# Performance work log

Hardware: AMD Instinct MI355X
Metric: run time of the kernel (lower is better)

The kernel has to match this reference:

```python
import jax, jax.numpy as jnp
import numpy as np

ALPHA = 0.5
PATH_LEN = 7  # 1 start entity + 3 (module, entity) hops
NUM_ENTITIES = 200000
EMBED = 128
NUM_MOD = 64
HIDDEN = 512
OUT_DIM = 64
BATCH = 8192


def setup_inputs() -> dict:
    key = jax.random.key(0)
    ks = jax.random.split(key, 8)
    stdv = 1.0 / np.sqrt(EMBED)
    return {
        "entity_embeds": jax.random.normal(ks[0], (NUM_ENTITIES, EMBED), jnp.float32) * 0.05,
        "W_mods": jax.random.uniform(ks[1], (NUM_MOD, EMBED, EMBED), jnp.float32, -stdv, stdv),
        "W1": jax.random.normal(ks[2], (HIDDEN, EMBED), jnp.float32) * stdv,
        "b1": jax.random.normal(ks[3], (HIDDEN,), jnp.float32) * 0.01,
        "W2": jax.random.normal(ks[4], (OUT_DIM, HIDDEN), jnp.float32) * (1.0 / np.sqrt(HIDDEN)),
        "b2": jax.random.normal(ks[5], (OUT_DIM,), jnp.float32) * 0.01,
        "entity_ids": jax.random.randint(ks[6], (BATCH, 4), 0, NUM_ENTITIES, jnp.int64 if jax.config.jax_enable_x64 else jnp.int32),
        "module_ids": jax.random.randint(ks[7], (BATCH, 3), 0, NUM_MOD, jnp.int64 if jax.config.jax_enable_x64 else jnp.int32),
    }


def reference(entity_embeds, W_mods, W1, b1, W2, b2, entity_ids, module_ids):
    # Batched version of ModuleNet.forward over a batch of fixed-length-7 paths.
    x = entity_embeds[entity_ids[:, 0]]  # [B, E] start entity embedding
    bias = x
    for h in range(3):  # hops over (module_id, entity_id) pairs
        Wm = W_mods[module_ids[:, h]]          # [B, E, E] per-row weight gather
        bias = entity_embeds[entity_ids[:, h + 1]]  # [B, E]
        x = jax.nn.relu(jnp.einsum('boi,bi->bo', Wm, x) + bias)
    w = 1.0 / (PATH_LEN * ALPHA)
    out = (1.0 - w) * bias + w * x  # [B, E]
    # classifier: Linear -> ReLU -> Linear
    h1 = jax.nn.relu(out @ W1.T + b1)
    logits = h1 @ W2.T + b2  # [B, OUT_DIM]
    return logits
```

## Files before the change

kernel.cpp:

```cpp
#include <hip/hip_runtime.h>

namespace {

typedef short bf16x8 __attribute__((ext_vector_type(8)));
typedef float f32x4 __attribute__((ext_vector_type(4)));

constexpr int BATCH = 8192;
constexpr int NMOD  = 64;
constexpr int CAP   = 256;
constexpr int CSTR  = 16;
constexpr float WB  = 1.0f / (7.0f * 0.5f);

constexpr size_t OFF_XH0 = 0;
constexpr size_t OFF_XL0 = 524288;
constexpr size_t OFF_XH1 = 1048576;
constexpr size_t OFF_XL1 = 1572864;
constexpr size_t OFF_W1H = 2097152;
constexpr size_t OFF_W1L = 2129920;
constexpr size_t OFF_W2H = 2162688;
constexpr size_t OFF_W2L = 2179072;
constexpr size_t OFF_CNT = 2195456;
constexpr size_t OFF_BKT = 2198528;

__device__ __forceinline__ ushort f2bf(float x) {
  unsigned u = __builtin_bit_cast(unsigned, x);
  u += 0x7FFFu + ((u >> 16) & 1u);
  return (ushort)(u >> 16);
}
__device__ __forceinline__ float bf2f(ushort h) {
  return __builtin_bit_cast(float, ((unsigned)h) << 16);
}
__device__ __forceinline__ void cvt8(const float* v, bf16x8& hi, bf16x8& lo) {
#pragma unroll
  for (int j = 0; j < 8; ++j) {
    const float x = v[j];
    const ushort h = f2bf(x);
    hi[j] = (short)h;
    lo[j] = (short)f2bf(x - bf2f(h));
  }
}

__global__ __launch_bounds__(256) void k_prep(const float* __restrict__ W1,
                                              const float* __restrict__ W2,
                                              const int* __restrict__ mids,
                                              float* __restrict__ ws) {
  __shared__ int wsum[4];
  const int bx = blockIdx.x;
  const int tid = threadIdx.x;
  if (bx < 48) {
    const float* src;
    ushort *dh, *dl;
    size_t i8;
    if (bx < 32) {
      src = W1; dh = (ushort*)(ws + OFF_W1H); dl = (ushort*)(ws + OFF_W1L);
      i8 = (size_t)bx * 256 + tid;
    } else {
      src = W2; dh = (ushort*)(ws + OFF_W2H); dl = (ushort*)(ws + OFF_W2L);
      i8 = (size_t)(bx - 32) * 256 + tid;
    }
    float v[8];
    *(float4*)&v[0] = *(const float4*)&src[i8 * 8];
    *(float4*)&v[4] = *(const float4*)&src[i8 * 8 + 4];
    bf16x8 hi, lo;
    cvt8(v, hi, lo);
    *(bf16x8*)&dh[i8 * 8] = hi;
    *(bf16x8*)&dl[i8 * 8] = lo;
  } else {
    const int hm = bx - 48;
    const int h = hm >> 6, m = hm & 63;
    int* cnt = (int*)(ws + OFF_CNT);
    int* bkt = (int*)(ws + OFF_BKT) + hm * CAP;
    const int wv = tid >> 6, ln = tid & 63;
    int count = 0;
    for (int it = 0; it < BATCH / 256; ++it) {
      const int b = it * 256 + tid;
      const bool hit = (mids[b * 3 + h] == m);
      const unsigned long long mask = __ballot(hit);
      const int pre = __popcll(mask & ((1ull << ln) - 1ull));
      if (ln == 0) wsum[wv] = __popcll(mask);
      __syncthreads();
      int wbase = count;
#pragma unroll
      for (int u = 0; u < 4; ++u)
        if (u < wv) wbase += wsum[u];
      if (hit) bkt[wbase + pre] = b;
      count += wsum[0] + wsum[1] + wsum[2] + wsum[3];
      __syncthreads();
    }
    if (tid == 0) cnt[hm * CSTR] = count;
  }
}

template <int HOP>
__global__ __launch_bounds__(256, 2) void k_hop(const float* __restrict__ E,
                                                const float* __restrict__ Wm,
                                                const int* __restrict__ eids,
                                                float* __restrict__ ws) {
  const int m = blockIdx.x >> 2, sl = blockIdx.x & 3;
  const int cn = ((const int*)(ws + OFF_CNT))[(HOP * NMOD + m) * CSTR];
  const int r0 = sl * 64;
  if (r0 >= cn) return;
  const int nr = min(64, cn - r0);

  __shared__ ushort wh[128 * 72];
  __shared__ ushort wl[128 * 72];
  __shared__ int rows[64], esrc[64], ebia[64];

  const int tid = threadIdx.x;
  const float* WmG = Wm + (size_t)m * 16384;
  const int* bkt = (const int*)(ws + OFF_BKT) + (HOP * NMOD + m) * CAP + r0;
  const ushort* XHp = (const ushort*)(ws + (HOP == 2 ? OFF_XH1 : OFF_XH0));
  const ushort* XLp = (const ushort*)(ws + (HOP == 2 ? OFF_XL1 : OFF_XL0));
  ushort* XHn = (ushort*)(ws + (HOP == 1 ? OFF_XH1 : OFF_XH0));
  ushort* XLn = (ushort*)(ws + (HOP == 1 ? OFF_XL1 : OFF_XL0));

  if (tid < 64) {
    const int b = bkt[tid < nr ? tid : 0];
    rows[tid] = b;
    esrc[tid] = (HOP == 0) ? eids[b * 4] : b;
    ebia[tid] = eids[b * 4 + HOP + 1];
  }

  const int w = tid >> 6, l = tid & 63;
  const int lg = l >> 4, lr = l & 15;
  const int g0 = (w & 1) * 2, f0 = (w >> 1) * 4;

  f32x4 acc[2][4] = {};

#pragma unroll
  for (int p = 0; p < 2; ++p) {
    __syncthreads();
    for (int e = tid; e < 128 * 8; e += 256) {
      const int c = e >> 3, s = e & 7;
      float v[8];
      const float* sp = &WmG[(size_t)c * 128 + p * 64 + s * 8];
      *(float4*)&v[0] = *(const float4*)&sp[0];
      *(float4*)&v[4] = *(const float4*)&sp[4];
      bf16x8 hi, lo;
      cvt8(v, hi, lo);
      *(bf16x8*)&wh[c * 72 + s * 8] = hi;
      *(bf16x8*)&wl[c * 72 + s * 8] = lo;
    }
    __syncthreads();

    bf16x8 ah[2][2], al[2][2];
#pragma unroll
    for (int g = 0; g < 2; ++g) {
      const int row = (g0 + g) * 16 + lr;
#pragma unroll
      for (int s = 0; s < 2; ++s) {
        const int k0 = p * 64 + s * 32 + lg * 8;
        if (HOP == 0) {
          const float* sp = E + (size_t)esrc[row] * 128;
          float v[8];
          *(float4*)&v[0] = *(const float4*)&sp[k0];
          *(float4*)&v[4] = *(const float4*)&sp[k0 + 4];
          cvt8(v, ah[g][s], al[g][s]);
        } else {
          const size_t xo = (size_t)esrc[row] * 128 + k0;
          ah[g][s] = *(const bf16x8*)&XHp[xo];
          al[g][s] = *(const bf16x8*)&XLp[xo];
        }
      }
    }

#pragma unroll
    for (int f = 0; f < 4; ++f) {
      const int c = (f0 + f) * 16 + lr;
#pragma unroll
      for (int s = 0; s < 2; ++s) {
        const bf16x8 bh = *(const bf16x8*)&wh[c * 72 + s * 32 + lg * 8];
        const bf16x8 bl = *(const bf16x8*)&wl[c * 72 + s * 32 + lg * 8];
#pragma unroll
        for (int g = 0; g < 2; ++g) {
          acc[g][f] = __builtin_amdgcn_mfma_f32_16x16x32_bf16(ah[g][s], bh, acc[g][f], 0, 0, 0);
          acc[g][f] = __builtin_amdgcn_mfma_f32_16x16x32_bf16(al[g][s], bh, acc[g][f], 0, 0, 0);
          acc[g][f] = __builtin_amdgcn_mfma_f32_16x16x32_bf16(ah[g][s], bl, acc[g][f], 0, 0, 0);
        }
      }
    }
  }

#pragma unroll
  for (int g = 0; g < 2; ++g) {
#pragma unroll
    for (int q = 0; q < 4; ++q) {
      const int row = (g0 + g) * 16 + lg * 4 + q;
      if (row < nr) {
        const int b = rows[row];
        const float* bp = E + (size_t)ebia[row] * 128;
        const size_t ob = (size_t)b * 128;
#pragma unroll
        for (int f = 0; f < 4; ++f) {
          const int col = (f0 + f) * 16 + lr;
          const float bias = bp[col];
          float v = fmaxf(acc[g][f][q] + bias, 0.f);
          if (HOP == 2) v = (1.f - WB) * bias + WB * v;
          const ushort h = f2bf(v);
          XHn[ob + col] = h;
          XLn[ob + col] = f2bf(v - bf2f(h));
        }
      }
    }
  }
}

constexpr int HSTR = 520;
__global__ __launch_bounds__(256, 2) void k_mlp(const float* __restrict__ b1,
                                                const float* __restrict__ b2,
                                                float* __restrict__ ws,
                                                float* __restrict__ out) {
  __shared__ ushort hh[16 * HSTR];
  __shared__ ushort hl[16 * HSTR];
  const int tid = threadIdx.x;
  const int row0 = blockIdx.x * 16;
  const ushort* XH = (const ushort*)(ws + OFF_XH0);
  const ushort* XL = (const ushort*)(ws + OFF_XL0);
  const ushort* W1H = (const ushort*)(ws + OFF_W1H);
  const ushort* W1L = (const ushort*)(ws + OFF_W1L);
  const ushort* W2H = (const ushort*)(ws + OFF_W2H);
  const ushort* W2L = (const ushort*)(ws + OFF_W2L);

  const int w = tid >> 6, l = tid & 63;
  const int lg = l >> 4, lr = l & 15;

  bf16x8 ah[4], al[4];
#pragma unroll
  for (int s = 0; s < 4; ++s) {
    const size_t xo = (size_t)(row0 + lr) * 128 + s * 32 + lg * 8;
    ah[s] = *(const bf16x8*)&XH[xo];
    al[s] = *(const bf16x8*)&XL[xo];
  }
  f32x4 acc[8] = {};
#pragma unroll
  for (int f = 0; f < 8; ++f) {
    const int c = w * 128 + f * 16 + lr;
#pragma unroll
    for (int s = 0; s < 4; ++s) {
      const size_t wo = (size_t)c * 128 + s * 32 + lg * 8;
      const bf16x8 bh = *(const bf16x8*)&W1H[wo];
      const bf16x8 bl = *(const bf16x8*)&W1L[wo];
      acc[f] = __builtin_amdgcn_mfma_f32_16x16x32_bf16(ah[s], bh, acc[f], 0, 0, 0);
      acc[f] = __builtin_amdgcn_mfma_f32_16x16x32_bf16(al[s], bh, acc[f], 0, 0, 0);
      acc[f] = __builtin_amdgcn_mfma_f32_16x16x32_bf16(ah[s], bl, acc[f], 0, 0, 0);
    }
  }
#pragma unroll
  for (int f = 0; f < 8; ++f) {
    const int c = w * 128 + f * 16 + lr;
    const float bb = b1[c];
#pragma unroll
    for (int q = 0; q < 4; ++q) {
      const int r = lg * 4 + q;
      const float v = fmaxf(acc[f][q] + bb, 0.f);
      const ushort h = f2bf(v);
      hh[r * HSTR + c] = h;
      hl[r * HSTR + c] = f2bf(v - bf2f(h));
    }
  }
  __syncthreads();

  f32x4 acc2 = {};
#pragma unroll 4
  for (int s = 0; s < 16; ++s) {
    const size_t wo = (size_t)(w * 16 + lr) * 512 + s * 32 + lg * 8;
    const bf16x8 a2h = *(const bf16x8*)&W2H[wo];
    const bf16x8 a2l = *(const bf16x8*)&W2L[wo];
    const int ko = s * 32 + lg * 8;
    const bf16x8 b2h = *(const bf16x8*)&hh[lr * HSTR + ko];
    const bf16x8 b2l = *(const bf16x8*)&hl[lr * HSTR + ko];
    acc2 = __builtin_amdgcn_mfma_f32_16x16x32_bf16(a2h, b2h, acc2, 0, 0, 0);
    acc2 = __builtin_amdgcn_mfma_f32_16x16x32_bf16(a2l, b2h, acc2, 0, 0, 0);
    acc2 = __builtin_amdgcn_mfma_f32_16x16x32_bf16(a2h, b2l, acc2, 0, 0, 0);
  }
  const float4 bb2 = *(const float4*)&b2[w * 16 + lg * 4];
  float4 o;
  o.x = acc2[0] + bb2.x;
  o.y = acc2[1] + bb2.y;
  o.z = acc2[2] + bb2.z;
  o.w = acc2[3] + bb2.w;
  *(float4*)&out[(size_t)(row0 + lr) * 64 + w * 16 + lg * 4] = o;
}

}

extern "C" void kernel_launch(void* const* d_in, const int* in_sizes, int n_in,
                              void* d_out, int out_size, void* d_ws,
                              size_t ws_size, hipStream_t stream) {
  const float* E  = (const float*)d_in[0];
  const float* Wm = (const float*)d_in[1];
  const float* W1 = (const float*)d_in[2];
  const float* b1 = (const float*)d_in[3];
  const float* W2 = (const float*)d_in[4];
  const float* b2 = (const float*)d_in[5];
  const int* eids = (const int*)d_in[6];
  const int* mids = (const int*)d_in[7];
  float* out = (float*)d_out;
  float* ws = (float*)d_ws;

  k_prep<<<dim3(240), dim3(256), 0, stream>>>(W1, W2, mids, ws);
  k_hop<0><<<dim3(256), dim3(256), 0, stream>>>(E, Wm, eids, ws);
  k_hop<1><<<dim3(256), dim3(256), 0, stream>>>(E, Wm, eids, ws);
  k_hop<2><<<dim3(256), dim3(256), 0, stream>>>(E, Wm, eids, ws);
  k_mlp<<<dim3(512), dim3(256), 0, stream>>>(b1, b2, ws, out);
}
```

Before: 85.79 us.

## Pre-split module weights to bf16 hi/lo once and halve hop output columns per block

```diff
diff --git a/kernel.cpp b/kernel.cpp
--- a/kernel.cpp
+++ b/kernel.cpp
@@ -11,16 +11,18 @@
 constexpr int CSTR  = 16;
 constexpr float WB  = 1.0f / (7.0f * 0.5f);
 
-constexpr size_t OFF_XH0 = 0;
-constexpr size_t OFF_XL0 = 524288;
-constexpr size_t OFF_XH1 = 1048576;
-constexpr size_t OFF_XL1 = 1572864;
-constexpr size_t OFF_W1H = 2097152;
-constexpr size_t OFF_W1L = 2129920;
-constexpr size_t OFF_W2H = 2162688;
-constexpr size_t OFF_W2L = 2179072;
-constexpr size_t OFF_CNT = 2195456;
-constexpr size_t OFF_BKT = 2198528;
+constexpr size_t OFF_WMH = 0;
+constexpr size_t OFF_WML = 524288;
+constexpr size_t OFF_XH0 = 1048576;
+constexpr size_t OFF_XL0 = 1572864;
+constexpr size_t OFF_XH1 = 2097152;
+constexpr size_t OFF_XL1 = 2621440;
+constexpr size_t OFF_W1H = 3145728;
+constexpr size_t OFF_W1L = 3178496;
+constexpr size_t OFF_W2H = 3211264;
+constexpr size_t OFF_W2L = 3227648;
+constexpr size_t OFF_CNT = 3244032;
+constexpr size_t OFF_BKT = 3247104;
 
 __device__ __forceinline__ ushort f2bf(float x) {
   unsigned u = __builtin_bit_cast(unsigned, x);
@@ -40,23 +42,27 @@
   }
 }
 
-__global__ __launch_bounds__(256) void k_prep(const float* __restrict__ W1,
+__global__ __launch_bounds__(256) void k_prep(const float* __restrict__ Wm,
+                                              const float* __restrict__ W1,
                                               const float* __restrict__ W2,
                                               const int* __restrict__ mids,
                                               float* __restrict__ ws) {
   __shared__ int wsum[4];
   const int bx = blockIdx.x;
   const int tid = threadIdx.x;
-  if (bx < 48) {
+  if (bx < 560) {
     const float* src;
     ushort *dh, *dl;
     size_t i8;
-    if (bx < 32) {
+    if (bx < 512) {
+      src = Wm; dh = (ushort*)(ws + OFF_WMH); dl = (ushort*)(ws + OFF_WML);
+      i8 = (size_t)bx * 256 + tid;
+    } else if (bx < 544) {
       src = W1; dh = (ushort*)(ws + OFF_W1H); dl = (ushort*)(ws + OFF_W1L);
-      i8 = (size_t)bx * 256 + tid;
+      i8 = (size_t)(bx - 512) * 256 + tid;
     } else {
       src = W2; dh = (ushort*)(ws + OFF_W2H); dl = (ushort*)(ws + OFF_W2L);
-      i8 = (size_t)(bx - 32) * 256 + tid;
+      i8 = (size_t)(bx - 544) * 256 + tid;
     }
     float v[8];
     *(float4*)&v[0] = *(const float4*)&src[i8 * 8];
@@ -66,7 +72,7 @@
     *(bf16x8*)&dh[i8 * 8] = hi;
     *(bf16x8*)&dl[i8 * 8] = lo;
   } else {
-    const int hm = bx - 48;
+    const int hm = bx - 560;
     const int h = hm >> 6, m = hm & 63;
     int* cnt = (int*)(ws + OFF_CNT);
     int* bkt = (int*)(ws + OFF_BKT) + hm * CAP;
@@ -93,21 +99,22 @@
 
 template <int HOP>
 __global__ __launch_bounds__(256, 2) void k_hop(const float* __restrict__ E,
-                                                const float* __restrict__ Wm,
                                                 const int* __restrict__ eids,
                                                 float* __restrict__ ws) {
-  const int m = blockIdx.x >> 2, sl = blockIdx.x & 3;
+  const int m = blockIdx.x >> 3, sl = (blockIdx.x >> 1) & 3, ch = blockIdx.x & 1;
   const int cn = ((const int*)(ws + OFF_CNT))[(HOP * NMOD + m) * CSTR];
   const int r0 = sl * 64;
   if (r0 >= cn) return;
   const int nr = min(64, cn - r0);
-
-  __shared__ ushort wh[128 * 72];
-  __shared__ ushort wl[128 * 72];
+  const int c0 = ch * 64;
+
+  __shared__ ushort wh[64 * 72];
+  __shared__ ushort wl[64 * 72];
   __shared__ int rows[64], esrc[64], ebia[64];
 
   const int tid = threadIdx.x;
-  const float* WmG = Wm + (size_t)m * 16384;
+  const ushort* WhiG = (const ushort*)(ws + OFF_WMH) + (size_t)m * 16384;
+  const ushort* WloG = (const ushort*)(ws + OFF_WML) + (size_t)m * 16384;
   const int* bkt = (const int*)(ws + OFF_BKT) + (HOP * NMOD + m) * CAP + r0;
   const ushort* XHp = (const ushort*)(ws + (HOP == 2 ? OFF_XH1 : OFF_XH0));
   const ushort* XLp = (const ushort*)(ws + (HOP == 2 ? OFF_XL1 : OFF_XL0));
@@ -123,23 +130,18 @@
 
   const int w = tid >> 6, l = tid & 63;
   const int lg = l >> 4, lr = l & 15;
-  const int g0 = (w & 1) * 2, f0 = (w >> 1) * 4;
-
-  f32x4 acc[2][4] = {};
+  const int g0 = (w & 1) * 2, f0 = (w >> 1) * 2;
+
+  f32x4 acc[2][2] = {};
 
 #pragma unroll
   for (int p = 0; p < 2; ++p) {
     __syncthreads();
-    for (int e = tid; e < 128 * 8; e += 256) {
+    for (int e = tid; e < 64 * 8; e += 256) {
       const int c = e >> 3, s = e & 7;
-      float v[8];
-      const float* sp = &WmG[(size_t)c * 128 + p * 64 + s * 8];
-      *(float4*)&v[0] = *(const float4*)&sp[0];
-      *(float4*)&v[4] = *(const float4*)&sp[4];
-      bf16x8 hi, lo;
-      cvt8(v, hi, lo);
-      *(bf16x8*)&wh[c * 72 + s * 8] = hi;
-      *(bf16x8*)&wl[c * 72 + s * 8] = lo;
+      const size_t go = (size_t)(c0 + c) * 128 + p * 64 + s * 8;
+      *(bf16x8*)&wh[c * 72 + s * 8] = *(const bf16x8*)&WhiG[go];
+      *(bf16x8*)&wl[c * 72 + s * 8] = *(const bf16x8*)&WloG[go];
     }
     __syncthreads();
 
@@ -165,7 +167,7 @@
     }
 
 #pragma unroll
-    for (int f = 0; f < 4; ++f) {
+    for (int f = 0; f < 2; ++f) {
       const int c = (f0 + f) * 16 + lr;
 #pragma unroll
       for (int s = 0; s < 2; ++s) {
@@ -191,8 +193,8 @@
         const float* bp = E + (size_t)ebia[row] * 128;
         const size_t ob = (size_t)b * 128;
 #pragma unroll
-        for (int f = 0; f < 4; ++f) {
-          const int col = (f0 + f) * 16 + lr;
+        for (int f = 0; f < 2; ++f) {
+          const int col = c0 + (f0 + f) * 16 + lr;
           const float bias = bp[col];
           float v = fmaxf(acc[g][f][q] + bias, 0.f);
           if (HOP == 2) v = (1.f - WB) * bias + WB * v;
@@ -298,9 +300,9 @@
   float* out = (float*)d_out;
   float* ws = (float*)d_ws;
 
-  k_prep<<<dim3(240), dim3(256), 0, stream>>>(W1, W2, mids, ws);
-  k_hop<0><<<dim3(256), dim3(256), 0, stream>>>(E, Wm, eids, ws);
-  k_hop<1><<<dim3(256), dim3(256), 0, stream>>>(E, Wm, eids, ws);
-  k_hop<2><<<dim3(256), dim3(256), 0, stream>>>(E, Wm, eids, ws);
+  k_prep<<<dim3(752), dim3(256), 0, stream>>>(Wm, W1, W2, mids, ws);
+  k_hop<0><<<dim3(512), dim3(256), 0, stream>>>(E, eids, ws);
+  k_hop<1><<<dim3(512), dim3(256), 0, stream>>>(E, eids, ws);
+  k_hop<2><<<dim3(512), dim3(256), 0, stream>>>(E, eids, ws);
   k_mlp<<<dim3(512), dim3(256), 0, stream>>>(b1, b2, ws, out);
 }
```

Result: no change. 87.23 us (+1.7%).
